# Optimization experiments

Measured on AMD Instinct MI355X. Metric: run time of the kernel, lower is better.

Reference implementation:

```python
import jax, jax.numpy as jnp
import numpy as np

N_NODES = 100000
N_EDGES = 1600000
D_IN = 64
D_OUT = 64


def setup_inputs() -> dict:
    key = jax.random.key(0)
    k1, k2, k3, k4 = jax.random.split(key, 4)
    feat = jax.random.normal(k1, (N_NODES, D_IN), dtype=jnp.float32)
    edge_src = jax.random.randint(k2, (N_EDGES,), 0, N_NODES, dtype=jnp.int64)
    edge_dst = jax.random.randint(k3, (N_EDGES,), 0, N_NODES, dtype=jnp.int64)
    # xavier_uniform with gain for relu (sqrt(2)) on [out, in] Linear weight
    gain = float(np.sqrt(2.0))
    limit = gain * float(np.sqrt(6.0 / (D_IN + D_OUT)))
    fc_weight = jax.random.uniform(k4, (D_OUT, D_IN), dtype=jnp.float32,
                                   minval=-limit, maxval=limit)
    return {"feat": feat, "edge_src": edge_src, "edge_dst": edge_dst,
            "fc_weight": fc_weight}


def reference(feat, edge_src, edge_dst, fc_weight):
    # SDDMM: edge score a_e = <h_src, h_dst>  (fn.u_dot_v)
    h_src = feat[edge_src]                      # [E, d]
    h_dst = feat[edge_dst]                      # [E, d]
    a = jnp.sum(h_src * h_dst, axis=-1, keepdims=True)  # [E, 1]
    # SpMM: neigh[v] = sum_{(u->v)} h_u * a_e  (u_mul_e + sum)
    m = h_src * a                               # [E, d]
    neigh = jax.ops.segment_sum(m, edge_dst, num_segments=feat.shape[0])  # [N, d]
    # Linear without bias: y = neigh @ W.T
    return neigh @ fc_weight.T
```

## Files before the change

### kernel.cpp

```cpp
#include <hip/hip_runtime.h>

#define N_NODES 100000
#define N_EDGES 1600000
#define D 64
#define NB 782
#define CAP 3072
#define EPB 8192
#define NPART ((N_EDGES + EPB - 1) / EPB)

typedef unsigned short ushort_t;
typedef unsigned int uint_t;

__device__ __forceinline__ ushort_t f2bf(float f) {
    uint_t u = __float_as_uint(f);
    u += 0x7FFF + ((u >> 16) & 1);
    return (ushort_t)(u >> 16);
}

__global__ __launch_bounds__(256) void repack_init(const float* __restrict__ feat,
                                                   ushort_t* __restrict__ featb,
                                                   int* __restrict__ gcur) {
    const int tid = blockIdx.x * 256 + threadIdx.x;
    if (tid < NB) gcur[tid] = tid * CAP;
    const int base = tid * 16;
    if (base >= N_NODES * D) return;
    const float4* f4 = (const float4*)(feat + base);
    ushort4* o4 = (ushort4*)(featb + base);
#pragma unroll
    for (int j = 0; j < 4; ++j) {
        const float4 v = f4[j];
        o4[j] = make_ushort4(f2bf(v.x), f2bf(v.y), f2bf(v.z), f2bf(v.w));
    }
}

__global__ __launch_bounds__(512) void partition(const int* __restrict__ esrc,
                                                 const int* __restrict__ edst,
                                                 int* __restrict__ gcur,
                                                 int* __restrict__ slab) {
    __shared__ ushort_t stage[EPB];
    __shared__ int cnt[NB];
    __shared__ int start[NB];
    __shared__ int cur[NB];
    __shared__ int gb[NB];
    __shared__ int s[512];
    const int t = threadIdx.x;
    const int base = blockIdx.x * EPB;
    const int n = min(EPB, N_EDGES - base);

    for (int i = t; i < NB; i += 512) cnt[i] = 0;
    __syncthreads();
    for (int i = t; i < n; i += 512) atomicAdd(&cnt[edst[base + i] >> 7], 1);
    __syncthreads();
    int a = 0, b2 = 0;
    if (2 * t < NB) a = cnt[2 * t];
    if (2 * t + 1 < NB) b2 = cnt[2 * t + 1];
    const int sum = a + b2;
    s[t] = sum;
    __syncthreads();
    for (int off = 1; off < 512; off <<= 1) {
        const int x = (t >= off) ? s[t - off] : 0;
        __syncthreads();
        s[t] += x;
        __syncthreads();
    }
    const int excl = s[t] - sum;
    if (2 * t < NB)     { start[2 * t] = excl;          cur[2 * t] = excl; }
    if (2 * t + 1 < NB) { start[2 * t + 1] = excl + a;  cur[2 * t + 1] = excl + a; }
    __syncthreads();
    for (int k = t; k < NB; k += 512) {
        const int c = cnt[k];
        gb[k] = (c ? atomicAdd(&gcur[k], c) : 0) - start[k];
    }
    __syncthreads();
    for (int i = t; i < n; i += 512) {
        const int pos = atomicAdd(&cur[edst[base + i] >> 7], 1);
        stage[pos] = (ushort_t)i;
    }
    __syncthreads();
    for (int i = t; i < n; i += 512) {
        const int j = stage[i];
        const int d = edst[base + j];
        const int bkt = d >> 7;
        const int gp = gb[bkt] + i;
        if (gp < (bkt + 1) * CAP)
            slab[gp] = ((d & 127) << 17) | esrc[base + j];
    }
}

template<int CTRL>
__device__ __forceinline__ float fadd_dpp(float x) {
    const int r = __builtin_amdgcn_update_dpp(0, __float_as_int(x), CTRL, 0xF, 0xF, true);
    return x + __int_as_float(r);
}
__device__ __forceinline__ float red8(float p) {
    p = fadd_dpp<0xB1>(p);
    p = fadd_dpp<0x4E>(p);
    p = fadd_dpp<0x141>(p);
    return p;
}

__device__ __forceinline__ float cvt_dot(const uint4 u, const float* __restrict__ h,
                                         float* __restrict__ g) {
    g[0] = __uint_as_float(u.x << 16); g[1] = __uint_as_float(u.x & 0xFFFF0000u);
    g[2] = __uint_as_float(u.y << 16); g[3] = __uint_as_float(u.y & 0xFFFF0000u);
    g[4] = __uint_as_float(u.z << 16); g[5] = __uint_as_float(u.z & 0xFFFF0000u);
    g[6] = __uint_as_float(u.w << 16); g[7] = __uint_as_float(u.w & 0xFFFF0000u);
    float p = 0.f;
#pragma unroll
    for (int k = 0; k < 8; ++k) p += g[k] * h[k];
    return p;
}

__global__ __launch_bounds__(512) void fused_spmm(const float4* __restrict__ feat4,
                                                  const uint4* __restrict__ featb4,
                                                  const int* __restrict__ slab,
                                                  const int* __restrict__ gcur,
                                                  float4* __restrict__ neigh4) {
    __shared__ int se[CAP];
    __shared__ int cnt[128];
    __shared__ int rowoff[129];
    __shared__ int cur[128];
    const int t = threadIdx.x;
    const int b = blockIdx.x;
    const int nbase = b << 7;
    const int nb_nodes = min(128, N_NODES - nbase);
    const int sbase = b * CAP;
    const int ne = min(gcur[b] - sbase, CAP);

    if (t < 128) cnt[t] = 0;
    __syncthreads();
    for (int i = t; i < ne; i += 512)
        atomicAdd(&cnt[slab[sbase + i] >> 17], 1);
    __syncthreads();
    for (int off = 1; off < 128; off <<= 1) {
        const int x = (t >= off && t < 128) ? cnt[t - off] : 0;
        __syncthreads();
        if (t < 128) cnt[t] += x;
        __syncthreads();
    }
    if (t == 0) rowoff[0] = 0;
    if (t < 128) rowoff[t + 1] = cnt[t];
    __syncthreads();
    if (t < 128) cur[t] = rowoff[t];
    __syncthreads();
    for (int i = t; i < ne; i += 512) {
        const int pk = slab[sbase + i];
        const int pos = atomicAdd(&cur[pk >> 17], 1);
        se[pos] = pk & 0x1FFFF;
    }
    __syncthreads();

    const int slot = t >> 3;
    const int l = t & 7;
#pragma unroll
    for (int ln0 = 0; ln0 < 128; ln0 += 64) {
        const int ln = ln0 + slot;
        if (ln >= nb_nodes) continue;
        const int nidx = nbase + ln;
        float h[8];
        {
            const float4 ha = feat4[nidx * 16 + 2 * l];
            const float4 hb = feat4[nidx * 16 + 2 * l + 1];
            h[0] = ha.x; h[1] = ha.y; h[2] = ha.z; h[3] = ha.w;
            h[4] = hb.x; h[5] = hb.y; h[6] = hb.z; h[7] = hb.w;
        }
        float acc[8];
#pragma unroll
        for (int k = 0; k < 8; ++k) acc[k] = 0.f;

        int e = rowoff[ln];
        const int e1 = rowoff[ln + 1];
        for (; e + 3 < e1; e += 4) {
            const int s0 = se[e], s1 = se[e + 1], s2 = se[e + 2], s3 = se[e + 3];
            const uint4 u0 = featb4[s0 * 8 + l];
            const uint4 u1 = featb4[s1 * 8 + l];
            const uint4 u2 = featb4[s2 * 8 + l];
            const uint4 u3 = featb4[s3 * 8 + l];
            float g0[8], g1[8], g2[8], g3[8];
            float p0 = cvt_dot(u0, h, g0);
            float p1 = cvt_dot(u1, h, g1);
            float p2 = cvt_dot(u2, h, g2);
            float p3 = cvt_dot(u3, h, g3);
            p0 = red8(p0); p1 = red8(p1); p2 = red8(p2); p3 = red8(p3);
#pragma unroll
            for (int k = 0; k < 8; ++k)
                acc[k] += g0[k] * p0 + g1[k] * p1 + g2[k] * p2 + g3[k] * p3;
        }
        for (; e < e1; ++e) {
            const uint4 u0 = featb4[se[e] * 8 + l];
            float g0[8];
            float p0 = red8(cvt_dot(u0, h, g0));
#pragma unroll
            for (int k = 0; k < 8; ++k) acc[k] += g0[k] * p0;
        }
        neigh4[nidx * 16 + 2 * l]     = make_float4(acc[0], acc[1], acc[2], acc[3]);
        neigh4[nidx * 16 + 2 * l + 1] = make_float4(acc[4], acc[5], acc[6], acc[7]);
    }
}

__global__ __launch_bounds__(256) void gemm_inplace(float* __restrict__ out,
                                                    const float* __restrict__ W) {
    __shared__ float WT[64][68];
    __shared__ float nT[64][132];
    const int t = threadIdx.x;

    const float4* W4 = (const float4*)W;
#pragma unroll
    for (int j = 0; j < 4; ++j) {
        const int f = t + j * 256;
        const int o = f >> 4;
        const int i4 = (f & 15) * 4;
        const float4 w = W4[f];
        WT[i4 + 0][o] = w.x;
        WT[i4 + 1][o] = w.y;
        WT[i4 + 2][o] = w.z;
        WT[i4 + 3][o] = w.w;
    }

    const int base = blockIdx.x * 128;
    const int rows = min(128, N_NODES - base);
    const float4* O4 = (const float4*)(out + (long)base * D);
#pragma unroll
    for (int j = 0; j < 8; ++j) {
        const int f = t + j * 256;
        const int r = f >> 4;
        const int i4 = (f & 15) * 4;
        if (r < rows) {
            const float4 x = O4[f];
            nT[i4 + 0][r] = x.x;
            nT[i4 + 1][r] = x.y;
            nT[i4 + 2][r] = x.z;
            nT[i4 + 3][r] = x.w;
        }
    }
    __syncthreads();

    const int c4 = (t & 15) * 4;
    const int r0 = (t >> 4) * 8;
    float acc[8][4];
#pragma unroll
    for (int r = 0; r < 8; ++r)
#pragma unroll
        for (int c = 0; c < 4; ++c) acc[r][c] = 0.f;

    for (int i = 0; i < 64; ++i) {
        const float4 w = *(const float4*)&WT[i][c4];
        const float4 ra = *(const float4*)&nT[i][r0];
        const float4 rb = *(const float4*)&nT[i][r0 + 4];
        const float wv[4] = {w.x, w.y, w.z, w.w};
        const float rv[8] = {ra.x, ra.y, ra.z, ra.w, rb.x, rb.y, rb.z, rb.w};
#pragma unroll
        for (int r = 0; r < 8; ++r)
#pragma unroll
            for (int c = 0; c < 4; ++c) acc[r][c] += rv[r] * wv[c];
    }

#pragma unroll
    for (int r = 0; r < 8; ++r) {
        const int rr = r0 + r;
        if (rr < rows)
            *(float4*)&out[(long)(base + rr) * D + c4] =
                make_float4(acc[r][0], acc[r][1], acc[r][2], acc[r][3]);
    }
}

extern "C" void kernel_launch(void* const* d_in, const int* in_sizes, int n_in,
                              void* d_out, int out_size, void* d_ws, size_t ws_size,
                              hipStream_t stream) {
    const float* feat = (const float*)d_in[0];
    const int*   esrc = (const int*)d_in[1];
    const int*   edst = (const int*)d_in[2];
    const float* W    = (const float*)d_in[3];
    float* out = (float*)d_out;

    char* ws = (char*)d_ws;
    ushort_t* featb = (ushort_t*)(ws);
    int* slab = (int*)(ws + 12800000);
    int* gcur = (int*)(ws + 12800000 + (size_t)NB * CAP * 4);

    repack_init<<<(N_NODES * D / 16 + 255) / 256, 256, 0, stream>>>(feat, featb, gcur);
    partition<<<NPART, 512, 0, stream>>>(esrc, edst, gcur, slab);
    fused_spmm<<<NB, 512, 0, stream>>>((const float4*)feat, (const uint4*)featb,
                                       slab, gcur, (float4*)out);
    gemm_inplace<<<(N_NODES + 127) / 128, 256, 0, stream>>>(out, W);
}
```

Before: 175.0 us.

## Sub-sort edges by source range within rows and stage partition records in LDS

The partition kernel now runs 1024 threads per block. It builds the packed (dst-low, src) record and the bucket id during the scatter into shared memory, so the final pass no longer re-reads edst and esrc from global memory through an indirection. The fused SpMM kernel copies its slab into LDS once and sorts each destination row's edges by the high bits of the source index (8 sub-buckets per row) using a 1024-entry counting sort. This groups the gather addresses in featb to improve cache locality. The cost is more LDS use, an extra scan over 1024 keys, and extra synchronization.

```diff
diff --git a/kernel.cpp b/kernel.cpp
--- a/kernel.cpp
+++ b/kernel.cpp
@@ -7,6 +7,7 @@
 #define CAP 3072
 #define EPB 8192
 #define NPART ((N_EDGES + EPB - 1) / EPB)
+#define RSH 14
 
 typedef unsigned short ushort_t;
 typedef unsigned int uint_t;
@@ -33,57 +34,53 @@
     }
 }
 
-__global__ __launch_bounds__(512) void partition(const int* __restrict__ esrc,
-                                                 const int* __restrict__ edst,
-                                                 int* __restrict__ gcur,
-                                                 int* __restrict__ slab) {
-    __shared__ ushort_t stage[EPB];
+__global__ __launch_bounds__(1024) void partition(const int* __restrict__ esrc,
+                                                  const int* __restrict__ edst,
+                                                  int* __restrict__ gcur,
+                                                  int* __restrict__ slab) {
+    __shared__ int stage[EPB];
+    __shared__ ushort_t bkt16[EPB];
     __shared__ int cnt[NB];
-    __shared__ int start[NB];
     __shared__ int cur[NB];
     __shared__ int gb[NB];
-    __shared__ int s[512];
+    __shared__ int s[1024];
     const int t = threadIdx.x;
     const int base = blockIdx.x * EPB;
     const int n = min(EPB, N_EDGES - base);
 
-    for (int i = t; i < NB; i += 512) cnt[i] = 0;
-    __syncthreads();
-    for (int i = t; i < n; i += 512) atomicAdd(&cnt[edst[base + i] >> 7], 1);
-    __syncthreads();
-    int a = 0, b2 = 0;
-    if (2 * t < NB) a = cnt[2 * t];
-    if (2 * t + 1 < NB) b2 = cnt[2 * t + 1];
-    const int sum = a + b2;
-    s[t] = sum;
-    __syncthreads();
-    for (int off = 1; off < 512; off <<= 1) {
+    if (t < NB) cnt[t] = 0;
+    __syncthreads();
+    for (int i = t; i < n; i += 1024)
+        atomicAdd(&cnt[edst[base + i] >> 7], 1);
+    __syncthreads();
+    const int v = (t < NB) ? cnt[t] : 0;
+    s[t] = v;
+    __syncthreads();
+    for (int off = 1; off < 1024; off <<= 1) {
         const int x = (t >= off) ? s[t - off] : 0;
         __syncthreads();
         s[t] += x;
         __syncthreads();
     }
-    const int excl = s[t] - sum;
-    if (2 * t < NB)     { start[2 * t] = excl;          cur[2 * t] = excl; }
-    if (2 * t + 1 < NB) { start[2 * t + 1] = excl + a;  cur[2 * t + 1] = excl + a; }
-    __syncthreads();
-    for (int k = t; k < NB; k += 512) {
-        const int c = cnt[k];
-        gb[k] = (c ? atomicAdd(&gcur[k], c) : 0) - start[k];
-    }
-    __syncthreads();
-    for (int i = t; i < n; i += 512) {
-        const int pos = atomicAdd(&cur[edst[base + i] >> 7], 1);
-        stage[pos] = (ushort_t)i;
-    }
-    __syncthreads();
-    for (int i = t; i < n; i += 512) {
-        const int j = stage[i];
-        const int d = edst[base + j];
+    if (t < NB) {
+        const int excl = s[t] - v;
+        cur[t] = excl;
+        gb[t] = (v ? atomicAdd(&gcur[t], v) : 0) - excl;
+    }
+    __syncthreads();
+    for (int i = t; i < n; i += 1024) {
+        const int d = edst[base + i];
         const int bkt = d >> 7;
+        const int pos = atomicAdd(&cur[bkt], 1);
+        stage[pos] = ((d & 127) << 17) | esrc[base + i];
+        bkt16[pos] = (ushort_t)bkt;
+    }
+    __syncthreads();
+    for (int i = t; i < n; i += 1024) {
+        const int bkt = bkt16[i];
         const int gp = gb[bkt] + i;
         if (gp < (bkt + 1) * CAP)
-            slab[gp] = ((d & 127) << 17) | esrc[base + j];
+            slab[gp] = stage[i];
     }
 }
 
@@ -116,10 +113,12 @@
                                                   const int* __restrict__ slab,
                                                   const int* __restrict__ gcur,
                                                   float4* __restrict__ neigh4) {
-    __shared__ int se[CAP];
-    __shared__ int cnt[128];
+    __shared__ int seA[CAP];
+    __shared__ int seB[CAP];
+    __shared__ int cnt[1024];
+    __shared__ int cur[1024];
     __shared__ int rowoff[129];
-    __shared__ int cur[128];
+    __shared__ int s[512];
     const int t = threadIdx.x;
     const int b = blockIdx.x;
     const int nbase = b << 7;
@@ -127,26 +126,36 @@
     const int sbase = b * CAP;
     const int ne = min(gcur[b] - sbase, CAP);
 
-    if (t < 128) cnt[t] = 0;
-    __syncthreads();
-    for (int i = t; i < ne; i += 512)
-        atomicAdd(&cnt[slab[sbase + i] >> 17], 1);
-    __syncthreads();
-    for (int off = 1; off < 128; off <<= 1) {
-        const int x = (t >= off && t < 128) ? cnt[t - off] : 0;
-        __syncthreads();
-        if (t < 128) cnt[t] += x;
-        __syncthreads();
-    }
-    if (t == 0) rowoff[0] = 0;
-    if (t < 128) rowoff[t + 1] = cnt[t];
-    __syncthreads();
-    if (t < 128) cur[t] = rowoff[t];
+    for (int i = t; i < ne; i += 512) seA[i] = slab[sbase + i];
+    cnt[t] = 0; cnt[t + 512] = 0;
     __syncthreads();
     for (int i = t; i < ne; i += 512) {
-        const int pk = slab[sbase + i];
-        const int pos = atomicAdd(&cur[pk >> 17], 1);
-        se[pos] = pk & 0x1FFFF;
+        const int pk = seA[i];
+        atomicAdd(&cnt[((pk >> 17) << 3) | ((pk & 0x1FFFF) >> RSH)], 1);
+    }
+    __syncthreads();
+    const int v0 = cnt[2 * t], v1 = cnt[2 * t + 1];
+    const int sum = v0 + v1;
+    s[t] = sum;
+    __syncthreads();
+    for (int off = 1; off < 512; off <<= 1) {
+        const int x = (t >= off) ? s[t - off] : 0;
+        __syncthreads();
+        s[t] += x;
+        __syncthreads();
+    }
+    const int excl = s[t] - sum;
+    cur[2 * t] = excl;
+    cur[2 * t + 1] = excl + v0;
+    __syncthreads();
+    if (t < 128) rowoff[t] = cur[t << 3];
+    if (t == 0) rowoff[128] = ne;
+    __syncthreads();
+    for (int i = t; i < ne; i += 512) {
+        const int pk = seA[i];
+        const int key = ((pk >> 17) << 3) | ((pk & 0x1FFFF) >> RSH);
+        const int pos = atomicAdd(&cur[key], 1);
+        seB[pos] = pk & 0x1FFFF;
     }
     __syncthreads();
 
@@ -171,7 +180,7 @@
         int e = rowoff[ln];
         const int e1 = rowoff[ln + 1];
         for (; e + 3 < e1; e += 4) {
-            const int s0 = se[e], s1 = se[e + 1], s2 = se[e + 2], s3 = se[e + 3];
+            const int s0 = seB[e], s1 = seB[e + 1], s2 = seB[e + 2], s3 = seB[e + 3];
             const uint4 u0 = featb4[s0 * 8 + l];
             const uint4 u1 = featb4[s1 * 8 + l];
             const uint4 u2 = featb4[s2 * 8 + l];
@@ -187,7 +196,7 @@
                 acc[k] += g0[k] * p0 + g1[k] * p1 + g2[k] * p2 + g3[k] * p3;
         }
         for (; e < e1; ++e) {
-            const uint4 u0 = featb4[se[e] * 8 + l];
+            const uint4 u0 = featb4[seB[e] * 8 + l];
             float g0[8];
             float p0 = red8(cvt_dot(u0, h, g0));
 #pragma unroll
@@ -279,7 +288,7 @@
     int* gcur = (int*)(ws + 12800000 + (size_t)NB * CAP * 4);
 
     repack_init<<<(N_NODES * D / 16 + 255) / 256, 256, 0, stream>>>(feat, featb, gcur);
-    partition<<<NPART, 512, 0, stream>>>(esrc, edst, gcur, slab);
+    partition<<<NPART, 1024, 0, stream>>>(esrc, edst, gcur, slab);
     fused_spmm<<<NB, 512, 0, stream>>>((const float4*)feat, (const uint4*)featb,
                                        slab, gcur, (float4*)out);
     gemm_inplace<<<(N_NODES + 127) / 128, 256, 0, stream>>>(out, W);
```

After: 168.9 us. 1.04x faster.
